# Kernel tuning notes

Hardware: AMD Instinct MI355X
Metric: run time of the kernel (lower is better)

The kernel has to match this reference:

```python
import jax, jax.numpy as jnp
import numpy as np

D = 1024
H = 16
HD = D // H
EPS = 1e-5
NEG = -1e20


def _layernorm(x, w, b):
    m = jnp.mean(x, axis=-1, keepdims=True)
    v = jnp.mean((x - m) ** 2, axis=-1, keepdims=True)
    return (x - m) * jax.lax.rsqrt(v + EPS) * w + b


def setup_inputs() -> dict:
    key = jax.random.key(0)
    ks = jax.random.split(key, 16)
    s = 0.02
    inp = {
        "X": jax.random.normal(ks[0], (2, 2048, D), jnp.float32),
        "Wq": jax.random.normal(ks[1], (D, D), jnp.float32) * s,
        "bq": jnp.zeros((D,), jnp.float32),
        "Wk": jax.random.normal(ks[2], (D, D), jnp.float32) * s,
        "bk": jnp.zeros((D,), jnp.float32),
        "Wv": jax.random.normal(ks[3], (D, D), jnp.float32) * s,
        "bv": jnp.zeros((D,), jnp.float32),
        "Wo": jax.random.normal(ks[4], (D, D), jnp.float32) * s,
        "bo": jnp.zeros((D,), jnp.float32),
        "ln1_w": jnp.ones((D,), jnp.float32),
        "ln1_b": jnp.zeros((D,), jnp.float32),
        "Wup": jax.random.normal(ks[5], (4 * D, D), jnp.float32) * s,
        "bup": jnp.zeros((4 * D,), jnp.float32),
        "Wdown": jax.random.normal(ks[6], (D, 4 * D), jnp.float32) * s,
        "bdown": jnp.zeros((D,), jnp.float32),
        "ln2_w": jnp.ones((D,), jnp.float32),
        "ln2_b": jnp.zeros((D,), jnp.float32),
    }
    return inp


def reference(X, Wq, bq, Wk, bk, Wv, bv, Wo, bo, ln1_w, ln1_b,
              Wup, bup, Wdown, bdown, ln2_w, ln2_b):
    B, S, _ = X.shape
    # QKV projections -> [B, H, S, HD]
    q = (X @ Wq.T + bq).reshape(B, S, H, HD).transpose(0, 2, 1, 3)
    k = (X @ Wk.T + bk).reshape(B, S, H, HD).transpose(0, 2, 1, 3)
    v = (X @ Wv.T + bv).reshape(B, S, H, HD).transpose(0, 2, 1, 3)
    scores = jnp.einsum("bhqd,bhkd->bhqk", q, k) / jnp.sqrt(jnp.float32(HD))
    causal = jnp.tril(jnp.ones((S, S), dtype=bool))  # mask==0 -> -1e20
    scores = jnp.where(causal, scores, jnp.float32(NEG))
    attn = jax.nn.softmax(scores, axis=-1)  # dropout is identity in eval
    out = jnp.einsum("bhqk,bhkd->bhqd", attn, v)
    out = out.transpose(0, 2, 1, 3).reshape(B, S, D)
    out = out @ Wo.T + bo
    x = _layernorm(X + out, ln1_w, ln1_b)  # post-LN attention block
    up = jax.nn.relu(x @ Wup.T + bup)
    down = up @ Wdown.T + bdown
    return _layernorm(x + down, ln2_w, ln2_b)
```

## Files before the change

### kernel.cpp

```cpp
#include <hip/hip_runtime.h>
#include <stdint.h>

#define DMODEL 1024
#define NHEAD 16
#define HDIM 64
#define SEQ 2048
#define NBATCH 2
#define MTOK 4096

typedef float f32x4 __attribute__((ext_vector_type(4)));
typedef short s16x8 __attribute__((ext_vector_type(8)));
typedef unsigned short u16;
typedef u16 u16x4 __attribute__((ext_vector_type(4)));

typedef __attribute__((address_space(1))) const void* as1_cvp;
typedef __attribute__((address_space(3))) void* as3_vp;

__device__ inline u16 f2bf(float f) {
  uint32_t u = __float_as_uint(f);
  u = u + 0x7FFFu + ((u >> 16) & 1u);
  return (u16)(u >> 16);
}

__device__ inline void gload_lds16(const void* g, void* l) {
  __builtin_amdgcn_global_load_lds((as1_cvp)g, (as3_vp)l, 16, 0, 0);
}

__global__ __launch_bounds__(256) void k_f2bf(const float* __restrict__ src,
                                              u16* __restrict__ dst, int n4) {
  int i = blockIdx.x * 256 + threadIdx.x;
  int stride = gridDim.x * 256;
  for (; i < n4; i += stride) {
    f32x4 v = ((const f32x4*)src)[i];
    u16x4 o;
    o[0] = f2bf(v[0]); o[1] = f2bf(v[1]); o[2] = f2bf(v[2]); o[3] = f2bf(v[3]);
    ((u16x4*)dst)[i] = o;
  }
}

__global__ __launch_bounds__(256) void k_f2bf_w4(
    const float* __restrict__ s0, const float* __restrict__ s1,
    const float* __restrict__ s2, const float* __restrict__ s3,
    u16* __restrict__ d0, u16* __restrict__ d1, u16* __restrict__ d2,
    u16* __restrict__ d3, int n4) {
  const float* src = blockIdx.y == 0 ? s0 : blockIdx.y == 1 ? s1
                     : blockIdx.y == 2 ? s2 : s3;
  u16* dst = blockIdx.y == 0 ? d0 : blockIdx.y == 1 ? d1
             : blockIdx.y == 2 ? d2 : d3;
  int i = blockIdx.x * 256 + threadIdx.x;
  int stride = gridDim.x * 256;
  for (; i < n4; i += stride) {
    f32x4 v = ((const f32x4*)src)[i];
    u16x4 o;
    o[0] = f2bf(v[0]); o[1] = f2bf(v[1]); o[2] = f2bf(v[2]); o[3] = f2bf(v[3]);
    ((u16x4*)dst)[i] = o;
  }
}

template <int MODE, int KSPL, int MH>
__global__ __launch_bounds__(512, 2) void k_gemm256(
    const u16* __restrict__ A, const u16* __restrict__ B,
    const float* __restrict__ bias, void* __restrict__ Cv,
    void* __restrict__ Cv1, int M, int N, int K) {
  constexpr int HALVES = MH + 2;
  __shared__ alignas(16) u16 lds[2 * HALVES * 8192];
  const int t = threadIdx.x;
  const int w = t >> 6;
  const int l = t & 63;
  const int wr = w >> 2;
  const int wc = w & 3;
  const int lr = l & 15, lg = l >> 4;
  const int r7 = lr & 7;
  const int lrow8 = l >> 3;

  const int gx = gridDim.x;
  int lin = blockIdx.y * gx + blockIdx.x;
  const int nwg = gx * gridDim.y;
  lin = (lin & 7) * (nwg >> 3) + (lin >> 3);
  const int bx = lin % gx, by = lin / gx;
  const int kz = KSPL > 1 ? blockIdx.z : 0;
  const int Kc = K / KSPL, kbeg = kz * Kc;
  const int brow = by * (MH * 128), bcol = bx * 256;

  constexpr int MF = MH * 4;
  const f32x4 Z4 = {0.f, 0.f, 0.f, 0.f};
  f32x4 acc[MF][4];
#pragma unroll
  for (int m = 0; m < MF; m++)
#pragma unroll
    for (int n = 0; n < 4; n++) acc[m][n] = Z4;

  const u16* Ag = A + (size_t)brow * K + kbeg;
  const u16* Bg = B + (size_t)bcol * K + kbeg;
  const int swz_src = ((l & 7) ^ ((l >> 3) & 7)) << 3;

  auto ldsH = [&](int buf, int half) { return lds + (buf * HALVES + half) * 8192; };
  auto stageA = [&](int kt, int buf) {
#pragma unroll
    for (int h = 0; h < MH; h++) {
      u16* lb = ldsH(buf, h);
      const int rb = h * 128;
      gload_lds16(Ag + (size_t)(rb + w * 8 + lrow8) * K + kt * 64 + swz_src,
                  lb + w * 512);
      gload_lds16(Ag + (size_t)(rb + 64 + w * 8 + lrow8) * K + kt * 64 + swz_src,
                  lb + (8 + w) * 512);
    }
  };
  auto stageB = [&](int kt, int buf) {
#pragma unroll
    for (int h = 0; h < 2; h++) {
      u16* lb = ldsH(buf, MH + h);
      const int rb = h * 128;
      gload_lds16(Bg + (size_t)(rb + w * 8 + lrow8) * K + kt * 64 + swz_src,
                  lb + w * 512);
      gload_lds16(Bg + (size_t)(rb + 64 + w * 8 + lrow8) * K + kt * 64 + swz_src,
                  lb + (8 + w) * 512);
    }
  };

  stageA(0, 0);
  stageB(0, 0);

  const int nkt = Kc >> 6;
  const int arb = (MH == 2) ? 0 : wr * 64;
  const int brb = (wc & 1) * 64;
  for (int kt = 0; kt < nkt; ++kt) {
    const int cur = kt & 1, nx = cur ^ 1;
    if (kt + 1 < nkt) {
      stageA(kt + 1, nx);
      if (MH == 2)
        asm volatile("s_waitcnt vmcnt(4)" ::: "memory");
      else
        asm volatile("s_waitcnt vmcnt(2)" ::: "memory");
    } else {
      asm volatile("s_waitcnt vmcnt(0)" ::: "memory");
    }
    __builtin_amdgcn_s_barrier();
    __builtin_amdgcn_sched_barrier(0);
    const u16* Ah = ldsH(cur, (MH == 2) ? wr : 0);
    const u16* Bh = ldsH(cur, MH + (wc >> 1));
#pragma unroll
    for (int kk = 0; kk < 2; kk++) {
      s16x8 bfr[4];
#pragma unroll
      for (int nf = 0; nf < 4; nf++)
        bfr[nf] = *(const s16x8*)(Bh + (brb + nf * 16 + lr) * 64 +
                                  (((kk * 4 + lg) ^ r7) << 3));
#pragma unroll
      for (int mh = 0; mh < MH; mh++) {
        s16x8 afr[4];
#pragma unroll
        for (int i = 0; i < 4; i++)
          afr[i] = *(const s16x8*)(Ah + (arb + (mh * 4 + i) * 16 + lr) * 64 +
                                   (((kk * 4 + lg) ^ r7) << 3));
        __builtin_amdgcn_s_setprio(1);
#pragma unroll
        for (int i = 0; i < 4; i++)
#pragma unroll
          for (int nf = 0; nf < 4; nf++)
            acc[mh * 4 + i][nf] = __builtin_amdgcn_mfma_f32_16x16x32_bf16(
                afr[i], bfr[nf], acc[mh * 4 + i][nf], 0, 0, 0);
        __builtin_amdgcn_s_setprio(0);
      }
      if (kk == 0 && kt + 1 < nkt) stageB(kt + 1, nx);
    }
    __builtin_amdgcn_sched_barrier(0);
    __builtin_amdgcn_s_barrier();
  }

  const int lg4 = lg * 4;
  const int wrb = wr * (MH == 2 ? 128 : 64);
  if (MODE == 0) {
    float* Co = (kz == 0) ? (float*)Cv : (float*)Cv1;
#pragma unroll
    for (int nf = 0; nf < 4; nf++) {
      const int col = bcol + wc * 64 + nf * 16 + lr;
      const float bvv = (kz == 0) ? bias[col] : 0.0f;
#pragma unroll
      for (int mf = 0; mf < MF; mf++) {
        const int row0 = brow + wrb + mf * 16 + lg4;
#pragma unroll
        for (int r = 0; r < 4; r++)
          Co[(size_t)(row0 + r) * N + col] = acc[mf][nf][r] + bvv;
      }
    }
  } else {
    u16* Sgw = lds + w * 2176;
    float bn[4];
#pragma unroll
    for (int nf = 0; nf < 4; nf++) bn[nf] = bias[bcol + wc * 64 + nf * 16 + lr];
    const int ch = l & 7;
#pragma unroll
    for (int hh = 0; hh < MH * 2; hh++) {
#pragma unroll
      for (int mm = 0; mm < 2; mm++) {
        const int mf = hh * 2 + mm;
#pragma unroll
        for (int nf = 0; nf < 4; nf++)
#pragma unroll
          for (int r = 0; r < 4; r++) {
            float vv = acc[mf][nf][r] + bn[nf];
            if (MODE == 2) vv = vv > 0.f ? vv : 0.f;
            Sgw[(mm * 16 + lg4 + r) * 68 + nf * 16 + lr] = f2bf(vv);
          }
      }
#pragma unroll
      for (int i = 0; i < 4; i++) {
        const int rr = i * 8 + (l >> 3);
        u16x4 a0 = *(const u16x4*)(Sgw + rr * 68 + ch * 8);
        u16x4 a1 = *(const u16x4*)(Sgw + rr * 68 + ch * 8 + 4);
        s16x8 v8;
#pragma unroll
        for (int j = 0; j < 4; j++) { v8[j] = (short)a0[j]; v8[4 + j] = (short)a1[j]; }
        *(s16x8*)((u16*)Cv + (size_t)(brow + wrb + hh * 32 + rr) * N +
                  (bcol + wc * 64 + ch * 8)) = v8;
      }
    }
  }
}

__global__ __launch_bounds__(512, 2) void k_gemm256_qkv(
    const u16* __restrict__ A, const u16* __restrict__ B,
    const float* __restrict__ bq, const float* __restrict__ bk,
    const float* __restrict__ bv, u16* __restrict__ qbf, u16* __restrict__ kbf,
    u16* __restrict__ vtbf, int M, int N, int K) {
  __shared__ alignas(16) u16 lds[2 * 3 * 8192];
  const int t = threadIdx.x;
  const int w = t >> 6, l = t & 63;
  const int wr = w >> 2, wc = w & 3;
  const int lr = l & 15, lg = l >> 4;
  const int r7 = lr & 7;
  const int lrow8 = l >> 3;

  const int gx = gridDim.x;
  int lin = blockIdx.y * gx + blockIdx.x;
  const int nwg = gx * gridDim.y;
  lin = (lin & 7) * (nwg >> 3) + (lin >> 3);
  const int bx = lin % gx, by = lin / gx;
  const int brow = by * 128, bcol = bx * 256;

  const f32x4 Z4 = {0.f, 0.f, 0.f, 0.f};
  f32x4 acc[4][4];
#pragma unroll
  for (int m = 0; m < 4; m++)
#pragma unroll
    for (int n = 0; n < 4; n++) acc[m][n] = Z4;

  const u16* Ag = A + (size_t)brow * K;
  const u16* Bg = B + (size_t)bcol * K;
  const int swz_src = ((l & 7) ^ ((l >> 3) & 7)) << 3;

  auto ldsH = [&](int buf, int half) { return lds + (buf * 3 + half) * 8192; };
  auto stageA = [&](int kt, int buf) {
    u16* lb = ldsH(buf, 0);
    gload_lds16(Ag + (size_t)(w * 8 + lrow8) * K + kt * 64 + swz_src,
                lb + w * 512);
    gload_lds16(Ag + (size_t)(64 + w * 8 + lrow8) * K + kt * 64 + swz_src,
                lb + (8 + w) * 512);
  };
  auto stageB = [&](int kt, int buf) {
#pragma unroll
    for (int h = 0; h < 2; h++) {
      u16* lb = ldsH(buf, 1 + h);
      const int rb = h * 128;
      gload_lds16(Bg + (size_t)(rb + w * 8 + lrow8) * K + kt * 64 + swz_src,
                  lb + w * 512);
      gload_lds16(Bg + (size_t)(rb + 64 + w * 8 + lrow8) * K + kt * 64 + swz_src,
                  lb + (8 + w) * 512);
    }
  };

  stageA(0, 0);
  stageB(0, 0);

  const int nkt = K >> 6;
  const int arb = wr * 64;
  const int brb = (wc & 1) * 64;
  for (int kt = 0; kt < nkt; ++kt) {
    const int cur = kt & 1, nx = cur ^ 1;
    if (kt + 1 < nkt) {
      stageA(kt + 1, nx);
      asm volatile("s_waitcnt vmcnt(2)" ::: "memory");
    } else {
      asm volatile("s_waitcnt vmcnt(0)" ::: "memory");
    }
    __builtin_amdgcn_s_barrier();
    __builtin_amdgcn_sched_barrier(0);
    const u16* Ah = ldsH(cur, 0);
    const u16* Bh = ldsH(cur, 1 + (wc >> 1));
#pragma unroll
    for (int kk = 0; kk < 2; kk++) {
      s16x8 bfr[4];
#pragma unroll
      for (int nf = 0; nf < 4; nf++)
        bfr[nf] = *(const s16x8*)(Bh + (brb + nf * 16 + lr) * 64 +
                                  (((kk * 4 + lg) ^ r7) << 3));
      s16x8 afr[4];
#pragma unroll
      for (int i = 0; i < 4; i++)
        afr[i] = *(const s16x8*)(Ah + (arb + i * 16 + lr) * 64 +
                                 (((kk * 4 + lg) ^ r7) << 3));
      __builtin_amdgcn_s_setprio(1);
#pragma unroll
      for (int i = 0; i < 4; i++)
#pragma unroll
        for (int nf = 0; nf < 4; nf++)
          acc[i][nf] = __builtin_amdgcn_mfma_f32_16x16x32_bf16(
              afr[i], bfr[nf], acc[i][nf], 0, 0, 0);
      __builtin_amdgcn_s_setprio(0);
      if (kk == 0 && kt + 1 < nkt) stageB(kt + 1, nx);
    }
    __builtin_amdgcn_sched_barrier(0);
    __builtin_amdgcn_s_barrier();
  }

  const int lg4 = lg * 4;
  const int wrb = wr * 64;
  u16* Sgw = lds + w * 2176;
  const int colw = bcol + wc * 64;
  const int region = colw >> 10;
  const int ck0 = colw & 1023;
  float bn[4];
  {
    const float* bb = region == 0 ? bq : region == 1 ? bk : bv;
#pragma unroll
    for (int nf = 0; nf < 4; nf++) bn[nf] = bb[ck0 + nf * 16 + lr];
  }
  const int ch = l & 7;
  if (region <= 1) {
#pragma unroll
    for (int hh = 0; hh < 2; hh++) {
#pragma unroll
      for (int mm = 0; mm < 2; mm++) {
        const int mf = hh * 2 + mm;
#pragma unroll
        for (int nf = 0; nf < 4; nf++)
#pragma unroll
          for (int r = 0; r < 4; r++) {
            float vv = acc[mf][nf][r] + bn[nf];
            if (region == 0) vv *= 0.125f;
            Sgw[(mm * 16 + lg4 + r) * 68 + nf * 16 + lr] = f2bf(vv);
          }
      }
#pragma unroll
      for (int i = 0; i < 4; i++) {
        const int rr = i * 8 + (l >> 3);
        u16x4 a0 = *(const u16x4*)(Sgw + rr * 68 + ch * 8);
        u16x4 a1 = *(const u16x4*)(Sgw + rr * 68 + ch * 8 + 4);
        s16x8 v8;
#pragma unroll
        for (int j = 0; j < 4; j++) { v8[j] = (short)a0[j]; v8[4 + j] = (short)a1[j]; }
        const int tok = brow + wrb + hh * 32 + rr;
        if (region == 0)
          *(s16x8*)(qbf + (size_t)tok * 1024 + ck0 + ch * 8) = v8;
        else
          *(s16x8*)(kbf + (size_t)tok * 1024 + ck0 + (((ch ^ tok) & 7) << 3)) =
              v8;
      }
    }
  } else {
    const int hcol = ck0 >> 6;
#pragma unroll
    for (int hh = 0; hh < 2; hh++) {
#pragma unroll
      for (int nn = 0; nn < 2; nn++) {
        const int nf = 2 * hh + nn;
#pragma unroll
        for (int mf = 0; mf < 4; mf++)
#pragma unroll
          for (int r = 0; r < 4; r++)
            Sgw[(nn * 16 + lr) * 68 + mf * 16 + lg4 + r] =
                f2bf(acc[mf][nf][r] + bn[nf]);
      }
#pragma unroll
      for (int i = 0; i < 4; i++) {
        const int rr = i * 8 + (l >> 3);
        u16x4 a0 = *(const u16x4*)(Sgw + rr * 68 + ch * 8);
        u16x4 a1 = *(const u16x4*)(Sgw + rr * 68 + ch * 8 + 4);
        s16x8 v8;
#pragma unroll
        for (int j = 0; j < 4; j++) { v8[j] = (short)a0[j]; v8[4 + j] = (short)a1[j]; }
        const int d = hh * 32 + rr;
        const int tokb = brow + wrb + ch * 8;
        const int b = tokb >> 11, s64b = tokb & 2047;
        const int ssb = (s64b & ~63) + ((((s64b >> 3) ^ d) & 7) << 3);
        *(s16x8*)(vtbf + ((size_t)((b << 4) + hcol) * 64 + d) * 2048 + ssb) = v8;
      }
    }
  }
}

__global__ __launch_bounds__(256, 2) void k_attn(const u16* __restrict__ q,
                                                 const u16* __restrict__ kk,
                                                 const u16* __restrict__ vt,
                                                 u16* __restrict__ o) {
  __shared__ alignas(16) u16 Ks[2][64 * 64];
  __shared__ alignas(16) u16 Vs[2][64 * 64];
  __shared__ alignas(16) u16 Ps[4 * 16 * 64];
  const int t = threadIdx.x;
  const int w = t >> 6;
  const int l = t & 63;
  const int idx = blockIdx.x;
  const int bh = idx & 31;
  const int p = idx >> 5;
  const int pm = p >> 3, pj = p & 7;
  const int qt = pm * 8 + ((pm & 1) ? (7 - pj) : pj);
  const int b = bh >> 4, h = bh & 15;
  const u16* qb = q + (size_t)b * SEQ * DMODEL + h * HDIM;
  const u16* kb = kk + (size_t)b * SEQ * DMODEL + h * HDIM;
  const u16* vb = vt + (size_t)((b * 16 + h) * 64) * SEQ;

  const int sr = t >> 3;
  const int sc = (t & 7) * 8;
  gload_lds16(qb + (size_t)(qt * 64 + sr) * DMODEL + sc, Ps + w * 512);
  gload_lds16(qb + (size_t)(qt * 64 + sr + 32) * DMODEL + sc,
              Ps + 2048 + w * 512);
  gload_lds16(kb + (size_t)sr * DMODEL + sc, &Ks[0][0] + w * 512);
  gload_lds16(kb + (size_t)(sr + 32) * DMODEL + sc, &Ks[0][0] + 2048 + w * 512);
  gload_lds16(vb + (size_t)sr * SEQ + sc, &Vs[0][0] + w * 512);
  gload_lds16(vb + (size_t)(sr + 32) * SEQ + sc, &Vs[0][0] + 2048 + w * 512);

  const int lr = l & 15, lg = l >> 4;
  const int key = lr & 7;
  const f32x4 Z4 = {0.f, 0.f, 0.f, 0.f};
  float m_l = -3.0e38f, l_l = 0.f;
  f32x4 oacc[4];
  for (int m = 0; m < 4; m++) oacc[m] = Z4;
  s16x8 bq0, bq1;
  u16* PsW = Ps + w * 1024;

  for (int jt = 0; jt <= qt; jt++) {
    const int cur = jt & 1;
    if (jt < qt) {
      const int nx = cur ^ 1;
      gload_lds16(kb + (size_t)((jt + 1) * 64 + sr) * DMODEL + sc,
                  &Ks[nx][0] + w * 512);
      gload_lds16(kb + (size_t)((jt + 1) * 64 + sr + 32) * DMODEL + sc,
                  &Ks[nx][0] + 2048 + w * 512);
      gload_lds16(vb + (size_t)sr * SEQ + (jt + 1) * 64 + sc,
                  &Vs[nx][0] + w * 512);
      gload_lds16(vb + (size_t)(sr + 32) * SEQ + (jt + 1) * 64 + sc,
                  &Vs[nx][0] + 2048 + w * 512);
      asm volatile("s_waitcnt vmcnt(4)" ::: "memory");
    } else {
      asm volatile("s_waitcnt vmcnt(0)" ::: "memory");
    }
    __builtin_amdgcn_s_barrier();
    __builtin_amdgcn_sched_barrier(0);
    const u16* Kc = &Ks[cur][0];
    const u16* Vc = &Vs[cur][0];
    if (jt == 0) {
      bq0 = *(const s16x8*)(Ps + (w * 16 + lr) * 64 + lg * 8);
      bq1 = *(const s16x8*)(Ps + (w * 16 + lr) * 64 + 32 + lg * 8);
    }
    f32x4 sacc[4];
    for (int m = 0; m < 4; m++) sacc[m] = Z4;
    for (int m = 0; m < 4; m++) {
      s16x8 ak0 = *(const s16x8*)(Kc + (m * 16 + lr) * 64 + ((lg ^ key) << 3));
      s16x8 ak1 =
          *(const s16x8*)(Kc + (m * 16 + lr) * 64 + (((4 | lg) ^ key) << 3));
      sacc[m] = __builtin_amdgcn_mfma_f32_16x16x32_bf16(ak0, bq0, sacc[m], 0, 0, 0);
      sacc[m] = __builtin_amdgcn_mfma_f32_16x16x32_bf16(ak1, bq1, sacc[m], 0, 0, 0);
    }
    if (jt == qt) {
      const int q_rel = w * 16 + lr;
      for (int m = 0; m < 4; m++)
        for (int r = 0; r < 4; r++)
          if (m * 16 + lg * 4 + r > q_rel) sacc[m][r] = -3.0e38f;
    }
    float mx[4];
    for (int m = 0; m < 4; m++)
      mx[m] = fmaxf(fmaxf(sacc[m][0], sacc[m][1]),
                    fmaxf(sacc[m][2], sacc[m][3]));
    float pmax = fmaxf(fmaxf(mx[0], mx[1]), fmaxf(mx[2], mx[3]));
    pmax = fmaxf(pmax, __shfl_xor(pmax, 16, 64));
    pmax = fmaxf(pmax, __shfl_xor(pmax, 32, 64));
    if (!__all(pmax - m_l <= 8.0f)) {
      const float m_new = fmaxf(m_l, pmax);
      const float alpha = __expf(m_l - m_new);
      m_l = m_new;
      l_l *= alpha;
      for (int m = 0; m < 4; m++)
        for (int r = 0; r < 4; r++) oacc[m][r] *= alpha;
    }
    float p_[4][4], sm[4];
    for (int m = 0; m < 4; m++) {
      for (int r = 0; r < 4; r++) p_[m][r] = __expf(sacc[m][r] - m_l);
      sm[m] = (p_[m][0] + p_[m][1]) + (p_[m][2] + p_[m][3]);
    }
    float rs = (sm[0] + sm[1]) + (sm[2] + sm[3]);
    rs += __shfl_xor(rs, 16, 64);
    rs += __shfl_xor(rs, 32, 64);
    l_l += rs;
    for (int m = 0; m < 4; m++)
      for (int pr = 0; pr < 2; pr++) {
        const uint32_t pk = (uint32_t)f2bf(p_[m][2 * pr]) |
                            ((uint32_t)f2bf(p_[m][2 * pr + 1]) << 16);
        const int kv0 = m * 16 + lg * 4 + 2 * pr;
        ((uint32_t*)PsW)[lr * 32 + (((kv0 >> 3) ^ key) << 2) +
                         ((kv0 >> 1) & 3)] = pk;
      }
    __builtin_amdgcn_sched_barrier(0);
    s16x8 bp0 = *(const s16x8*)(PsW + lr * 64 + ((lg ^ key) << 3));
    s16x8 bp1 = *(const s16x8*)(PsW + lr * 64 + (((4 | lg) ^ key) << 3));
    for (int m = 0; m < 4; m++) {
      s16x8 av0 = *(const s16x8*)(Vc + (m * 16 + lr) * 64 + ((lg ^ key) << 3));
      s16x8 av1 =
          *(const s16x8*)(Vc + (m * 16 + lr) * 64 + (((4 | lg) ^ key) << 3));
      oacc[m] = __builtin_amdgcn_mfma_f32_16x16x32_bf16(av0, bp0, oacc[m], 0, 0, 0);
      oacc[m] = __builtin_amdgcn_mfma_f32_16x16x32_bf16(av1, bp1, oacc[m], 0, 0, 0);
    }
    __builtin_amdgcn_sched_barrier(0);
    __builtin_amdgcn_s_barrier();
  }
  const float rl = 1.0f / l_l;
  const int tok = qt * 64 + w * 16 + lr;
  u16* orow = o + (size_t)(b * SEQ + tok) * DMODEL + h * HDIM;
  for (int m = 0; m < 4; m++)
    for (int pr = 0; pr < 2; pr++) {
      const uint32_t pk = (uint32_t)f2bf(oacc[m][2 * pr] * rl) |
                          ((uint32_t)f2bf(oacc[m][2 * pr + 1] * rl) << 16);
      *(uint32_t*)(orow + m * 16 + lg * 4 + 2 * pr) = pk;
    }
}

__global__ __launch_bounds__(256) void k_add_ln(const float* __restrict__ X,
                                                const float* __restrict__ Y,
                                                const float* __restrict__ Y1,
                                                const float* __restrict__ w,
                                                const float* __restrict__ bias,
                                                float* __restrict__ of32,
                                                u16* __restrict__ obf) {
  __shared__ float sred[4];
  const int t = threadIdx.x;
  const size_t row = blockIdx.x;
  f32x4 xv = ((const f32x4*)(X + row * DMODEL))[t];
  f32x4 yv = ((const f32x4*)(Y + row * DMODEL))[t];
  f32x4 vv;
  for (int i = 0; i < 4; i++) vv[i] = xv[i] + yv[i];
  if (Y1) {
    f32x4 y1 = ((const f32x4*)(Y1 + row * DMODEL))[t];
    for (int i = 0; i < 4; i++) vv[i] += y1[i];
  }
  float s = vv[0] + vv[1] + vv[2] + vv[3];
  for (int off = 32; off >= 1; off >>= 1) s += __shfl_xor(s, off, 64);
  if ((t & 63) == 0) sred[t >> 6] = s;
  __syncthreads();
  s = sred[0] + sred[1] + sred[2] + sred[3];
  const float mean = s * (1.0f / DMODEL);
  f32x4 dv;
  for (int i = 0; i < 4; i++) dv[i] = vv[i] - mean;
  float ss = dv[0] * dv[0] + dv[1] * dv[1] + dv[2] * dv[2] + dv[3] * dv[3];
  __syncthreads();
  for (int off = 32; off >= 1; off >>= 1) ss += __shfl_xor(ss, off, 64);
  if ((t & 63) == 0) sred[t >> 6] = ss;
  __syncthreads();
  ss = sred[0] + sred[1] + sred[2] + sred[3];
  const float rs = rsqrtf(ss * (1.0f / DMODEL) + 1e-5f);
  f32x4 wv = ((const f32x4*)w)[t];
  f32x4 bv = ((const f32x4*)bias)[t];
  f32x4 ov;
  for (int i = 0; i < 4; i++) ov[i] = dv[i] * rs * wv[i] + bv[i];
  if (of32) ((f32x4*)(of32 + row * DMODEL))[t] = ov;
  if (obf) {
    u16x4 ob;
    for (int i = 0; i < 4; i++) ob[i] = f2bf(ov[i]);
    ((u16x4*)(obf + row * DMODEL))[t] = ob;
  }
}

extern "C" void kernel_launch(void* const* d_in, const int* in_sizes, int n_in,
                              void* d_out, int out_size, void* d_ws,
                              size_t ws_size, hipStream_t stream) {
  const float* X = (const float*)d_in[0];
  const float* Wq = (const float*)d_in[1];
  const float* bq = (const float*)d_in[2];
  const float* Wk = (const float*)d_in[3];
  const float* bk = (const float*)d_in[4];
  const float* Wv = (const float*)d_in[5];
  const float* bvp = (const float*)d_in[6];
  const float* Wo = (const float*)d_in[7];
  const float* bo = (const float*)d_in[8];
  const float* ln1w = (const float*)d_in[9];
  const float* ln1b = (const float*)d_in[10];
  const float* Wup = (const float*)d_in[11];
  const float* bup = (const float*)d_in[12];
  const float* Wdown = (const float*)d_in[13];
  const float* bdown = (const float*)d_in[14];
  const float* ln2w = (const float*)d_in[15];
  const float* ln2b = (const float*)d_in[16];

  char* ws = (char*)d_ws;
  const size_t MB = 1024 * 1024;
  u16* Xbf = (u16*)(ws + 0);
  u16* qbf = (u16*)(ws + 8 * MB);
  u16* kbf = (u16*)(ws + 16 * MB);
  u16* vtbf = (u16*)(ws + 24 * MB);
  u16* wqkv = (u16*)(ws + 32 * MB);
  u16* wo = (u16*)(ws + 38 * MB);
  u16* attnb = (u16*)(ws + 40 * MB);
  float* Ybuf = (float*)(ws + 48 * MB);
  float* xres = (float*)(ws + 64 * MB);
  u16* xbf = (u16*)(ws + 80 * MB);
  u16* upbf = (u16*)(ws + 0);
  u16* wbig = (u16*)(ws + 32 * MB);
  float* Ypart = (float*)d_out;

  const dim3 blk(256);
  k_f2bf<<<2048, blk, 0, stream>>>(X, Xbf, (MTOK * DMODEL) / 4);
  k_f2bf_w4<<<dim3(512, 4), blk, 0, stream>>>(
      Wq, Wk, Wv, Wo, wqkv + 0 * 1024 * 1024, wqkv + 1 * 1024 * 1024,
      wqkv + 2 * 1024 * 1024, wo, (DMODEL * DMODEL) / 4);

  k_gemm256_qkv<<<dim3(12, 32), dim3(512), 0, stream>>>(
      Xbf, wqkv, bq, bk, bvp, qbf, kbf, vtbf, MTOK, 3 * DMODEL, DMODEL);
  k_attn<<<NBATCH * NHEAD * (SEQ / 64), blk, 0, stream>>>(qbf, kbf, vtbf, attnb);
  k_gemm256<0, 2, 1><<<dim3(4, 32, 2), dim3(512), 0, stream>>>(
      attnb, wo, bo, Ybuf, Ypart, MTOK, DMODEL, DMODEL);
  k_add_ln<<<MTOK, blk, 0, stream>>>(X, Ybuf, Ypart, ln1w, ln1b, xres, xbf);

  k_f2bf<<<2048, blk, 0, stream>>>(Wup, wbig, (4 * DMODEL * DMODEL) / 4);
  k_gemm256<2, 1, 2><<<dim3(16, 16), dim3(512), 0, stream>>>(
      xbf, wbig, bup, upbf, nullptr, MTOK, 4 * DMODEL, DMODEL);
  k_f2bf<<<2048, blk, 0, stream>>>(Wdown, wbig, (4 * DMODEL * DMODEL) / 4);
  k_gemm256<0, 2, 1><<<dim3(4, 32, 2), dim3(512), 0, stream>>>(
      upbf, wbig, bdown, Ybuf, Ypart, MTOK, DMODEL, 4 * DMODEL);
  k_add_ln<<<MTOK, blk, 0, stream>>>(xres, Ybuf, Ypart, ln2w, ln2b,
                                     (float*)d_out, (u16*)nullptr);
}
```

Measured before the change: 220.9 us.

## Enlarge QKV GEMM tile to 256x256 and pair causal attention query tiles per block

```diff
diff --git a/kernel.cpp b/kernel.cpp
--- a/kernel.cpp
+++ b/kernel.cpp
@@ -20,6 +20,12 @@
   uint32_t u = __float_as_uint(f);
   u = u + 0x7FFFu + ((u >> 16) & 1u);
   return (u16)(u >> 16);
+}
+
+__device__ inline uint32_t pk_bf16(float lo, float hi) {
+  uint32_t r;
+  asm("v_cvt_pk_bf16_f32 %0, %1, %2" : "=v"(r) : "v"(lo), "v"(hi));
+  return r;
 }
 
 __device__ inline void gload_lds16(const void* g, void* l) {
@@ -224,7 +230,7 @@
     const float* __restrict__ bq, const float* __restrict__ bk,
     const float* __restrict__ bv, u16* __restrict__ qbf, u16* __restrict__ kbf,
     u16* __restrict__ vtbf, int M, int N, int K) {
-  __shared__ alignas(16) u16 lds[2 * 3 * 8192];
+  __shared__ alignas(16) u16 lds[2 * 4 * 8192];
   const int t = threadIdx.x;
   const int w = t >> 6, l = t & 63;
   const int wr = w >> 2, wc = w & 3;
@@ -237,12 +243,12 @@
   const int nwg = gx * gridDim.y;
   lin = (lin & 7) * (nwg >> 3) + (lin >> 3);
   const int bx = lin % gx, by = lin / gx;
-  const int brow = by * 128, bcol = bx * 256;
+  const int brow = by * 256, bcol = bx * 256;
 
   const f32x4 Z4 = {0.f, 0.f, 0.f, 0.f};
-  f32x4 acc[4][4];
-#pragma unroll
-  for (int m = 0; m < 4; m++)
+  f32x4 acc[8][4];
+#pragma unroll
+  for (int m = 0; m < 8; m++)
 #pragma unroll
     for (int n = 0; n < 4; n++) acc[m][n] = Z4;
 
@@ -250,18 +256,22 @@
   const u16* Bg = B + (size_t)bcol * K;
   const int swz_src = ((l & 7) ^ ((l >> 3) & 7)) << 3;
 
-  auto ldsH = [&](int buf, int half) { return lds + (buf * 3 + half) * 8192; };
+  auto ldsH = [&](int buf, int half) { return lds + (buf * 4 + half) * 8192; };
   auto stageA = [&](int kt, int buf) {
-    u16* lb = ldsH(buf, 0);
-    gload_lds16(Ag + (size_t)(w * 8 + lrow8) * K + kt * 64 + swz_src,
-                lb + w * 512);
-    gload_lds16(Ag + (size_t)(64 + w * 8 + lrow8) * K + kt * 64 + swz_src,
-                lb + (8 + w) * 512);
+#pragma unroll
+    for (int h = 0; h < 2; h++) {
+      u16* lb = ldsH(buf, h);
+      const int rb = h * 128;
+      gload_lds16(Ag + (size_t)(rb + w * 8 + lrow8) * K + kt * 64 + swz_src,
+                  lb + w * 512);
+      gload_lds16(Ag + (size_t)(rb + 64 + w * 8 + lrow8) * K + kt * 64 + swz_src,
+                  lb + (8 + w) * 512);
+    }
   };
   auto stageB = [&](int kt, int buf) {
 #pragma unroll
     for (int h = 0; h < 2; h++) {
-      u16* lb = ldsH(buf, 1 + h);
+      u16* lb = ldsH(buf, 2 + h);
       const int rb = h * 128;
       gload_lds16(Bg + (size_t)(rb + w * 8 + lrow8) * K + kt * 64 + swz_src,
                   lb + w * 512);
@@ -274,20 +284,19 @@
   stageB(0, 0);
 
   const int nkt = K >> 6;
-  const int arb = wr * 64;
   const int brb = (wc & 1) * 64;
   for (int kt = 0; kt < nkt; ++kt) {
     const int cur = kt & 1, nx = cur ^ 1;
     if (kt + 1 < nkt) {
       stageA(kt + 1, nx);
-      asm volatile("s_waitcnt vmcnt(2)" ::: "memory");
+      asm volatile("s_waitcnt vmcnt(4)" ::: "memory");
     } else {
       asm volatile("s_waitcnt vmcnt(0)" ::: "memory");
     }
     __builtin_amdgcn_s_barrier();
     __builtin_amdgcn_sched_barrier(0);
-    const u16* Ah = ldsH(cur, 0);
-    const u16* Bh = ldsH(cur, 1 + (wc >> 1));
+    const u16* Ah = ldsH(cur, wr);
+    const u16* Bh = ldsH(cur, 2 + (wc >> 1));
 #pragma unroll
     for (int kk = 0; kk < 2; kk++) {
       s16x8 bfr[4];
@@ -295,19 +304,22 @@
       for (int nf = 0; nf < 4; nf++)
         bfr[nf] = *(const s16x8*)(Bh + (brb + nf * 16 + lr) * 64 +
                                   (((kk * 4 + lg) ^ r7) << 3));
-      s16x8 afr[4];
-#pragma unroll
-      for (int i = 0; i < 4; i++)
-        afr[i] = *(const s16x8*)(Ah + (arb + i * 16 + lr) * 64 +
-                                 (((kk * 4 + lg) ^ r7) << 3));
-      __builtin_amdgcn_s_setprio(1);
-#pragma unroll
-      for (int i = 0; i < 4; i++)
-#pragma unroll
-        for (int nf = 0; nf < 4; nf++)
-          acc[i][nf] = __builtin_amdgcn_mfma_f32_16x16x32_bf16(
-              afr[i], bfr[nf], acc[i][nf], 0, 0, 0);
-      __builtin_amdgcn_s_setprio(0);
+#pragma unroll
+      for (int mh = 0; mh < 2; mh++) {
+        s16x8 afr[4];
+#pragma unroll
+        for (int i = 0; i < 4; i++)
+          afr[i] = *(const s16x8*)(Ah + ((mh * 4 + i) * 16 + lr) * 64 +
+                                   (((kk * 4 + lg) ^ r7) << 3));
+        __builtin_amdgcn_s_setprio(1);
+#pragma unroll
+        for (int i = 0; i < 4; i++)
+#pragma unroll
+          for (int nf = 0; nf < 4; nf++)
+            acc[mh * 4 + i][nf] = __builtin_amdgcn_mfma_f32_16x16x32_bf16(
+                afr[i], bfr[nf], acc[mh * 4 + i][nf], 0, 0, 0);
+        __builtin_amdgcn_s_setprio(0);
+      }
       if (kk == 0 && kt + 1 < nkt) stageB(kt + 1, nx);
     }
     __builtin_amdgcn_sched_barrier(0);
@@ -315,7 +327,7 @@
   }
 
   const int lg4 = lg * 4;
-  const int wrb = wr * 64;
+  const int wrb = wr * 128;
   u16* Sgw = lds + w * 2176;
   const int colw = bcol + wc * 64;
   const int region = colw >> 10;
@@ -329,7 +341,7 @@
   const int ch = l & 7;
   if (region <= 1) {
 #pragma unroll
-    for (int hh = 0; hh < 2; hh++) {
+    for (int hh = 0; hh < 4; hh++) {
 #pragma unroll
       for (int mm = 0; mm < 2; mm++) {
         const int mf = hh * 2 + mm;
@@ -361,32 +373,37 @@
   } else {
     const int hcol = ck0 >> 6;
 #pragma unroll
-    for (int hh = 0; hh < 2; hh++) {
-#pragma unroll
-      for (int nn = 0; nn < 2; nn++) {
-        const int nf = 2 * hh + nn;
-#pragma unroll
-        for (int mf = 0; mf < 4; mf++)
-#pragma unroll
-          for (int r = 0; r < 4; r++)
-            Sgw[(nn * 16 + lr) * 68 + mf * 16 + lg4 + r] =
-                f2bf(acc[mf][nf][r] + bn[nf]);
-      }
-#pragma unroll
-      for (int i = 0; i < 4; i++) {
-        const int rr = i * 8 + (l >> 3);
-        u16x4 a0 = *(const u16x4*)(Sgw + rr * 68 + ch * 8);
-        u16x4 a1 = *(const u16x4*)(Sgw + rr * 68 + ch * 8 + 4);
-        s16x8 v8;
-#pragma unroll
-        for (int j = 0; j < 4; j++) { v8[j] = (short)a0[j]; v8[4 + j] = (short)a1[j]; }
-        const int d = hh * 32 + rr;
-        const int tokb = brow + wrb + ch * 8;
-        const int b = tokb >> 11, s64b = tokb & 2047;
-        const int ssb = (s64b & ~63) + ((((s64b >> 3) ^ d) & 7) << 3);
-        *(s16x8*)(vtbf + ((size_t)((b << 4) + hcol) * 64 + d) * 2048 + ssb) = v8;
-      }
-    }
+    for (int dh = 0; dh < 2; dh++)
+#pragma unroll
+      for (int th = 0; th < 2; th++) {
+#pragma unroll
+        for (int nn = 0; nn < 2; nn++) {
+          const int nf = dh * 2 + nn;
+#pragma unroll
+          for (int mi = 0; mi < 4; mi++) {
+            const int mf = th * 4 + mi;
+#pragma unroll
+            for (int r = 0; r < 4; r++)
+              Sgw[(nn * 16 + lr) * 68 + mi * 16 + lg4 + r] =
+                  f2bf(acc[mf][nf][r] + bn[nf]);
+          }
+        }
+#pragma unroll
+        for (int i = 0; i < 4; i++) {
+          const int rr = i * 8 + (l >> 3);
+          u16x4 a0 = *(const u16x4*)(Sgw + rr * 68 + ch * 8);
+          u16x4 a1 = *(const u16x4*)(Sgw + rr * 68 + ch * 8 + 4);
+          s16x8 v8;
+#pragma unroll
+          for (int j = 0; j < 4; j++) { v8[j] = (short)a0[j]; v8[4 + j] = (short)a1[j]; }
+          const int d = dh * 32 + rr;
+          const int tokb = brow + wrb + th * 64 + ch * 8;
+          const int b = tokb >> 11, s64b = tokb & 2047;
+          const int ssb = (s64b & ~63) + ((((s64b >> 3) ^ d) & 7) << 3);
+          *(s16x8*)(vtbf + ((size_t)((b << 4) + hcol) * 64 + d) * 2048 + ssb) =
+              v8;
+        }
+      }
   }
 }
 
@@ -403,8 +420,6 @@
   const int idx = blockIdx.x;
   const int bh = idx & 31;
   const int p = idx >> 5;
-  const int pm = p >> 3, pj = p & 7;
-  const int qt = pm * 8 + ((pm & 1) ? (7 - pj) : pj);
   const int b = bh >> 4, h = bh & 15;
   const u16* qb = q + (size_t)b * SEQ * DMODEL + h * HDIM;
   const u16* kb = kk + (size_t)b * SEQ * DMODEL + h * HDIM;
@@ -412,116 +427,122 @@
 
   const int sr = t >> 3;
   const int sc = (t & 7) * 8;
-  gload_lds16(qb + (size_t)(qt * 64 + sr) * DMODEL + sc, Ps + w * 512);
-  gload_lds16(qb + (size_t)(qt * 64 + sr + 32) * DMODEL + sc,
-              Ps + 2048 + w * 512);
-  gload_lds16(kb + (size_t)sr * DMODEL + sc, &Ks[0][0] + w * 512);
-  gload_lds16(kb + (size_t)(sr + 32) * DMODEL + sc, &Ks[0][0] + 2048 + w * 512);
-  gload_lds16(vb + (size_t)sr * SEQ + sc, &Vs[0][0] + w * 512);
-  gload_lds16(vb + (size_t)(sr + 32) * SEQ + sc, &Vs[0][0] + 2048 + w * 512);
-
   const int lr = l & 15, lg = l >> 4;
   const int key = lr & 7;
   const f32x4 Z4 = {0.f, 0.f, 0.f, 0.f};
-  float m_l = -3.0e38f, l_l = 0.f;
-  f32x4 oacc[4];
-  for (int m = 0; m < 4; m++) oacc[m] = Z4;
-  s16x8 bq0, bq1;
   u16* PsW = Ps + w * 1024;
 
-  for (int jt = 0; jt <= qt; jt++) {
-    const int cur = jt & 1;
-    if (jt < qt) {
-      const int nx = cur ^ 1;
-      gload_lds16(kb + (size_t)((jt + 1) * 64 + sr) * DMODEL + sc,
-                  &Ks[nx][0] + w * 512);
-      gload_lds16(kb + (size_t)((jt + 1) * 64 + sr + 32) * DMODEL + sc,
-                  &Ks[nx][0] + 2048 + w * 512);
-      gload_lds16(vb + (size_t)sr * SEQ + (jt + 1) * 64 + sc,
-                  &Vs[nx][0] + w * 512);
-      gload_lds16(vb + (size_t)(sr + 32) * SEQ + (jt + 1) * 64 + sc,
-                  &Vs[nx][0] + 2048 + w * 512);
-      asm volatile("s_waitcnt vmcnt(4)" ::: "memory");
-    } else {
-      asm volatile("s_waitcnt vmcnt(0)" ::: "memory");
-    }
-    __builtin_amdgcn_s_barrier();
-    __builtin_amdgcn_sched_barrier(0);
-    const u16* Kc = &Ks[cur][0];
-    const u16* Vc = &Vs[cur][0];
-    if (jt == 0) {
-      bq0 = *(const s16x8*)(Ps + (w * 16 + lr) * 64 + lg * 8);
-      bq1 = *(const s16x8*)(Ps + (w * 16 + lr) * 64 + 32 + lg * 8);
-    }
-    f32x4 sacc[4];
-    for (int m = 0; m < 4; m++) sacc[m] = Z4;
-    for (int m = 0; m < 4; m++) {
-      s16x8 ak0 = *(const s16x8*)(Kc + (m * 16 + lr) * 64 + ((lg ^ key) << 3));
-      s16x8 ak1 =
-          *(const s16x8*)(Kc + (m * 16 + lr) * 64 + (((4 | lg) ^ key) << 3));
-      sacc[m] = __builtin_amdgcn_mfma_f32_16x16x32_bf16(ak0, bq0, sacc[m], 0, 0, 0);
-      sacc[m] = __builtin_amdgcn_mfma_f32_16x16x32_bf16(ak1, bq1, sacc[m], 0, 0, 0);
-    }
-    if (jt == qt) {
-      const int q_rel = w * 16 + lr;
+  for (int half = 0; half < 2; half++) {
+    const int qt = half ? (31 - p) : p;
+    gload_lds16(qb + (size_t)(qt * 64 + sr) * DMODEL + sc, Ps + w * 512);
+    gload_lds16(qb + (size_t)(qt * 64 + sr + 32) * DMODEL + sc,
+                Ps + 2048 + w * 512);
+    gload_lds16(kb + (size_t)sr * DMODEL + sc, &Ks[0][0] + w * 512);
+    gload_lds16(kb + (size_t)(sr + 32) * DMODEL + sc,
+                &Ks[0][0] + 2048 + w * 512);
+    gload_lds16(vb + (size_t)sr * SEQ + sc, &Vs[0][0] + w * 512);
+    gload_lds16(vb + (size_t)(sr + 32) * SEQ + sc, &Vs[0][0] + 2048 + w * 512);
+
+    float m_l = -3.0e38f, l_l = 0.f;
+    f32x4 oacc[4];
+    for (int m = 0; m < 4; m++) oacc[m] = Z4;
+    s16x8 bq0, bq1;
+
+    for (int jt = 0; jt <= qt; jt++) {
+      const int cur = jt & 1;
+      if (jt < qt) {
+        const int nx = cur ^ 1;
+        gload_lds16(kb + (size_t)((jt + 1) * 64 + sr) * DMODEL + sc,
+                    &Ks[nx][0] + w * 512);
+        gload_lds16(kb + (size_t)((jt + 1) * 64 + sr + 32) * DMODEL + sc,
+                    &Ks[nx][0] + 2048 + w * 512);
+        gload_lds16(vb + (size_t)sr * SEQ + (jt + 1) * 64 + sc,
+                    &Vs[nx][0] + w * 512);
+        gload_lds16(vb + (size_t)(sr + 32) * SEQ + (jt + 1) * 64 + sc,
+                    &Vs[nx][0] + 2048 + w * 512);
+        asm volatile("s_waitcnt vmcnt(4)" ::: "memory");
+      } else {
+        asm volatile("s_waitcnt vmcnt(0)" ::: "memory");
+      }
+      __builtin_amdgcn_s_barrier();
+      __builtin_amdgcn_sched_barrier(0);
+      const u16* Kc = &Ks[cur][0];
+      const u16* Vc = &Vs[cur][0];
+      if (jt == 0) {
+        bq0 = *(const s16x8*)(Ps + (w * 16 + lr) * 64 + lg * 8);
+        bq1 = *(const s16x8*)(Ps + (w * 16 + lr) * 64 + 32 + lg * 8);
+      }
+      f32x4 sacc[4];
+      for (int m = 0; m < 4; m++) sacc[m] = Z4;
+      for (int m = 0; m < 4; m++) {
+        s16x8 ak0 =
+            *(const s16x8*)(Kc + (m * 16 + lr) * 64 + ((lg ^ key) << 3));
+        s16x8 ak1 =
+            *(const s16x8*)(Kc + (m * 16 + lr) * 64 + (((4 | lg) ^ key) << 3));
+        sacc[m] = __builtin_amdgcn_mfma_f32_16x16x32_bf16(ak0, bq0, sacc[m], 0, 0, 0);
+        sacc[m] = __builtin_amdgcn_mfma_f32_16x16x32_bf16(ak1, bq1, sacc[m], 0, 0, 0);
+      }
+      if (jt == qt) {
+        const int q_rel = w * 16 + lr;
+        for (int m = 0; m < 4; m++)
+          for (int r = 0; r < 4; r++)
+            if (m * 16 + lg * 4 + r > q_rel) sacc[m][r] = -3.0e38f;
+      }
+      float mx[4];
       for (int m = 0; m < 4; m++)
-        for (int r = 0; r < 4; r++)
-          if (m * 16 + lg * 4 + r > q_rel) sacc[m][r] = -3.0e38f;
-    }
-    float mx[4];
-    for (int m = 0; m < 4; m++)
-      mx[m] = fmaxf(fmaxf(sacc[m][0], sacc[m][1]),
-                    fmaxf(sacc[m][2], sacc[m][3]));
-    float pmax = fmaxf(fmaxf(mx[0], mx[1]), fmaxf(mx[2], mx[3]));
-    pmax = fmaxf(pmax, __shfl_xor(pmax, 16, 64));
-    pmax = fmaxf(pmax, __shfl_xor(pmax, 32, 64));
-    if (!__all(pmax - m_l <= 8.0f)) {
-      const float m_new = fmaxf(m_l, pmax);
-      const float alpha = __expf(m_l - m_new);
-      m_l = m_new;
-      l_l *= alpha;
+        mx[m] = fmaxf(fmaxf(sacc[m][0], sacc[m][1]),
+                      fmaxf(sacc[m][2], sacc[m][3]));
+      float pmax = fmaxf(fmaxf(mx[0], mx[1]), fmaxf(mx[2], mx[3]));
+      pmax = fmaxf(pmax, __shfl_xor(pmax, 16, 64));
+      pmax = fmaxf(pmax, __shfl_xor(pmax, 32, 64));
+      if (!__all(pmax - m_l <= 8.0f)) {
+        const float m_new = fmaxf(m_l, pmax);
+        const float alpha = __expf(m_l - m_new);
+        m_l = m_new;
+        l_l *= alpha;
+        for (int m = 0; m < 4; m++)
+          for (int r = 0; r < 4; r++) oacc[m][r] *= alpha;
+      }
+      float p_[4][4], sm[4];
+      for (int m = 0; m < 4; m++) {
+        for (int r = 0; r < 4; r++) p_[m][r] = __expf(sacc[m][r] - m_l);
+        sm[m] = (p_[m][0] + p_[m][1]) + (p_[m][2] + p_[m][3]);
+      }
+      float rs = (sm[0] + sm[1]) + (sm[2] + sm[3]);
+      rs += __shfl_xor(rs, 16, 64);
+      rs += __shfl_xor(rs, 32, 64);
+      l_l += rs;
       for (int m = 0; m < 4; m++)
-        for (int r = 0; r < 4; r++) oacc[m][r] *= alpha;
-    }
-    float p_[4][4], sm[4];
-    for (int m = 0; m < 4; m++) {
-      for (int r = 0; r < 4; r++) p_[m][r] = __expf(sacc[m][r] - m_l);
-      sm[m] = (p_[m][0] + p_[m][1]) + (p_[m][2] + p_[m][3]);
-    }
-    float rs = (sm[0] + sm[1]) + (sm[2] + sm[3]);
-    rs += __shfl_xor(rs, 16, 64);
-    rs += __shfl_xor(rs, 32, 64);
-    l_l += rs;
+        for (int pr = 0; pr < 2; pr++) {
+          const uint32_t pk = pk_bf16(p_[m][2 * pr], p_[m][2 * pr + 1]);
+          const int kv0 = m * 16 + lg * 4 + 2 * pr;
+          ((uint32_t*)PsW)[lr * 32 + (((kv0 >> 3) ^ key) << 2) +
+                           ((kv0 >> 1) & 3)] = pk;
+        }
+      __builtin_amdgcn_sched_barrier(0);
+      s16x8 bp0 = *(const s16x8*)(PsW + lr * 64 + ((lg ^ key) << 3));
+      s16x8 bp1 = *(const s16x8*)(PsW + lr * 64 + (((4 | lg) ^ key) << 3));
+      for (int m = 0; m < 4; m++) {
+        s16x8 av0 =
+            *(const s16x8*)(Vc + (m * 16 + lr) * 64 + ((lg ^ key) << 3));
+        s16x8 av1 =
+            *(const s16x8*)(Vc + (m * 16 + lr) * 64 + (((4 | lg) ^ key) << 3));
+        oacc[m] = __builtin_amdgcn_mfma_f32_16x16x32_bf16(av0, bp0, oacc[m], 0, 0, 0);
+        oacc[m] = __builtin_amdgcn_mfma_f32_16x16x32_bf16(av1, bp1, oacc[m], 0, 0, 0);
+      }
+      __builtin_amdgcn_sched_barrier(0);
+      __builtin_amdgcn_s_barrier();
+    }
+    const float rl = 1.0f / l_l;
+    const int tok = qt * 64 + w * 16 + lr;
+    u16* orow = o + (size_t)(b * SEQ + tok) * DMODEL + h * HDIM;
     for (int m = 0; m < 4; m++)
       for (int pr = 0; pr < 2; pr++) {
-        const uint32_t pk = (uint32_t)f2bf(p_[m][2 * pr]) |
-                            ((uint32_t)f2bf(p_[m][2 * pr + 1]) << 16);
-        const int kv0 = m * 16 + lg * 4 + 2 * pr;
-        ((uint32_t*)PsW)[lr * 32 + (((kv0 >> 3) ^ key) << 2) +
-                         ((kv0 >> 1) & 3)] = pk;
-      }
-    __builtin_amdgcn_sched_barrier(0);
-    s16x8 bp0 = *(const s16x8*)(PsW + lr * 64 + ((lg ^ key) << 3));
-    s16x8 bp1 = *(const s16x8*)(PsW + lr * 64 + (((4 | lg) ^ key) << 3));
-    for (int m = 0; m < 4; m++) {
-      s16x8 av0 = *(const s16x8*)(Vc + (m * 16 + lr) * 64 + ((lg ^ key) << 3));
-      s16x8 av1 =
-          *(const s16x8*)(Vc + (m * 16 + lr) * 64 + (((4 | lg) ^ key) << 3));
-      oacc[m] = __builtin_amdgcn_mfma_f32_16x16x32_bf16(av0, bp0, oacc[m], 0, 0, 0);
-      oacc[m] = __builtin_amdgcn_mfma_f32_16x16x32_bf16(av1, bp1, oacc[m], 0, 0, 0);
-    }
-    __builtin_amdgcn_sched_barrier(0);
-    __builtin_amdgcn_s_barrier();
-  }
-  const float rl = 1.0f / l_l;
-  const int tok = qt * 64 + w * 16 + lr;
-  u16* orow = o + (size_t)(b * SEQ + tok) * DMODEL + h * HDIM;
-  for (int m = 0; m < 4; m++)
-    for (int pr = 0; pr < 2; pr++) {
-      const uint32_t pk = (uint32_t)f2bf(oacc[m][2 * pr] * rl) |
-                          ((uint32_t)f2bf(oacc[m][2 * pr + 1] * rl) << 16);
-      *(uint32_t*)(orow + m * 16 + lg * 4 + 2 * pr) = pk;
-    }
+        const uint32_t pk =
+            pk_bf16(oacc[m][2 * pr] * rl, oacc[m][2 * pr + 1] * rl);
+        *(uint32_t*)(orow + m * 16 + lg * 4 + 2 * pr) = pk;
+      }
+  }
 }
 
 __global__ __launch_bounds__(256) void k_add_ln(const float* __restrict__ X,
@@ -612,9 +633,9 @@
       Wq, Wk, Wv, Wo, wqkv + 0 * 1024 * 1024, wqkv + 1 * 1024 * 1024,
       wqkv + 2 * 1024 * 1024, wo, (DMODEL * DMODEL) / 4);
 
-  k_gemm256_qkv<<<dim3(12, 32), dim3(512), 0, stream>>>(
+  k_gemm256_qkv<<<dim3(12, 16), dim3(512), 0, stream>>>(
       Xbf, wqkv, bq, bk, bvp, qbf, kbf, vtbf, MTOK, 3 * DMODEL, DMODEL);
-  k_attn<<<NBATCH * NHEAD * (SEQ / 64), blk, 0, stream>>>(qbf, kbf, vtbf, attnb);
+  k_attn<<<16 * NBATCH * NHEAD, blk, 0, stream>>>(qbf, kbf, vtbf, attnb);
   k_gemm256<0, 2, 1><<<dim3(4, 32, 2), dim3(512), 0, stream>>>(
       attnb, wo, bo, Ybuf, Ypart, MTOK, DMODEL, DMODEL);
   k_add_ln<<<MTOK, blk, 0, stream>>>(X, Ybuf, Ypart, ln1w, ln1b, xres, xbf);
```

Measured after the change: 211.2 us. 1.05x faster.
